# Performance work log

Measured on AMD Instinct MI355X. Metric: run time of the kernel, lower is better.

The kernel has to match this reference:

```python
import jax, jax.numpy as jnp
import numpy as np

K = 32

def leaky(v):
    return jnp.where(v >= 0, v, 0.2 * v)

def knn_cl(x, k):
    # x: [B,N,C] channel-last; returns idx [B,N,k] of k nearest (incl. self)
    xx = jnp.sum(x * x, axis=-1)                      # [B,N]
    inner = jnp.einsum('bnc,bmc->bnm', x, x)          # [B,N,N]
    pd = 2.0 * inner - xx[:, :, None] - xx[:, None, :]  # -squared dist
    return jax.lax.top_k(pd, k)[1]

def gfeat(x, k, knn_src=None):
    # x: [B,N,C] -> [B,N,k,2C] = cat(neighbor - center, center)
    idx = knn_cl(x if knn_src is None else knn_src, k)
    nb = jax.vmap(lambda f, i: f[i])(x, idx)          # [B,N,k,C]
    ctr = x[:, :, None, :]
    return jnp.concatenate([nb - ctr, jnp.broadcast_to(ctr, nb.shape)], axis=-1)

def block2(f, w, s, b):
    # 1x1 Conv2d + (folded) BN + LeakyReLU, channel-last [B,N,k,Cin]->[B,N,k,Cout]
    return leaky(jnp.einsum('bnkc,oc->bnko', f, w) * s + b)

def block1(f, w, s, b):
    # 1x1 Conv1d + (folded) BN + LeakyReLU, [B,N,Cin]->[B,N,Cout]
    return leaky(jnp.einsum('bnc,oc->bno', f, w) * s + b)

def setup_inputs() -> dict:
    key = jax.random.key(0)
    ks = jax.random.split(key, 32)
    B, C, N = 4, 8, 4096
    d = {}
    d['x'] = jax.random.normal(ks[0], (B, C, N), dtype=jnp.float32)
    wshapes = {'w1': (64, 16), 'w2': (64, 64), 'w3': (64, 128), 'w4': (64, 64),
               'w5': (64, 128), 'w6': (1024, 192), 'w7': (512, 1216),
               'w8': (256, 512), 'w9': (2, 256)}
    for i, (name, sh) in enumerate(wshapes.items()):
        d[name] = jax.random.normal(ks[1 + i], sh, dtype=jnp.float32) * 0.05
    bnsizes = [64, 64, 64, 64, 64, 1024, 512, 256]
    for i, c in enumerate(bnsizes):
        d['s%d' % (i + 1)] = jax.random.uniform(ks[10 + 2 * i], (c,), dtype=jnp.float32) + 0.5
        d['b%d' % (i + 1)] = jax.random.normal(ks[11 + 2 * i], (c,), dtype=jnp.float32) * 0.1
    return d

def reference(x, w1, w2, w3, w4, w5, w6, w7, w8, w9,
              s1, b1, s2, b2, s3, b3, s4, b4, s5, b5, s6, b6, s7, b7, s8, b8):
    B, _, N = x.shape
    xcl = jnp.transpose(x, (0, 2, 1))                 # [B,N,8]
    # EdgeConv block 1 (knn on channels 6: -> dim9=True path)
    f = gfeat(xcl, K, knn_src=xcl[..., 6:])           # [B,N,K,16]
    f = block2(f, w1, s1, b1)
    f = block2(f, w2, s2, b2)
    x1 = jnp.max(f, axis=2)                           # [B,N,64]
    # EdgeConv block 2
    f = gfeat(x1, K)                                  # [B,N,K,128]
    f = block2(f, w3, s3, b3)
    f = block2(f, w4, s4, b4)
    x2 = jnp.max(f, axis=2)                           # [B,N,64]
    # EdgeConv block 3
    f = gfeat(x2, K)                                  # [B,N,K,128]
    f = block2(f, w5, s5, b5)
    x3 = jnp.max(f, axis=2)                           # [B,N,64]
    cat = jnp.concatenate([x1, x2, x3], axis=-1)      # [B,N,192]
    g = block1(cat, w6, s6, b6)                       # [B,N,1024]
    g = jnp.broadcast_to(jnp.max(g, axis=1, keepdims=True), (B, N, 1024))
    h = jnp.concatenate([g, x1, x2, x3], axis=-1)     # [B,N,1216]
    h = block1(h, w7, s7, b7)                         # [B,N,512]
    h = block1(h, w8, s8, b8)                         # [B,N,256] (dropout is eval-mode identity)
    logits = jnp.einsum('bnc,oc->bno', h, w9)         # [B,N,2]
    return jnp.transpose(jax.nn.softmax(logits, axis=-1), (0, 2, 1))  # [B,2,N]
```

## Files before the change

### kernel.cpp

```cpp
#include <hip/hip_runtime.h>
#include <cstddef>

#define BATCH 4
#define NPTS 4096
#define KNN 32

__device__ __forceinline__ float leaky(float v) { return v >= 0.f ? v : 0.2f * v; }

__device__ __forceinline__ unsigned encf(float f) {
    unsigned b = __float_as_uint(f);
    return (b & 0x80000000u) ? ~b : (b | 0x80000000u);
}
__device__ __forceinline__ float decf(unsigned e) {
    unsigned b = (e & 0x80000000u) ? (e ^ 0x80000000u) : ~e;
    return __uint_as_float(b);
}
__device__ __forceinline__ unsigned umaxu(unsigned a, unsigned b) { return a > b ? a : b; }

__device__ __forceinline__ unsigned wave_umax_bcast(unsigned v) {
    int x = (int)v, t;
    t = __builtin_amdgcn_update_dpp(0, x, 0x111, 0xF, 0xF, true); x = (int)umaxu((unsigned)x, (unsigned)t);
    t = __builtin_amdgcn_update_dpp(0, x, 0x112, 0xF, 0xF, true); x = (int)umaxu((unsigned)x, (unsigned)t);
    t = __builtin_amdgcn_update_dpp(0, x, 0x114, 0xF, 0xF, true); x = (int)umaxu((unsigned)x, (unsigned)t);
    t = __builtin_amdgcn_update_dpp(0, x, 0x118, 0xF, 0xF, true); x = (int)umaxu((unsigned)x, (unsigned)t);
    t = __builtin_amdgcn_update_dpp(0, x, 0x142, 0xA, 0xF, true); x = (int)umaxu((unsigned)x, (unsigned)t);
    t = __builtin_amdgcn_update_dpp(0, x, 0x143, 0xC, 0xF, true); x = (int)umaxu((unsigned)x, (unsigned)t);
    return (unsigned)__builtin_amdgcn_readlane(x, 63);
}

template <int CM>
__device__ __forceinline__ void extract_step_reg(unsigned* u, unsigned* g, int lane,
                                                 int* __restrict__ outp, int it) {
    unsigned m8 = umaxu(umaxu(umaxu(g[0], g[1]), umaxu(g[2], g[3])),
                        umaxu(umaxu(g[4], g[5]), umaxu(g[6], g[7])));
    unsigned wm = wave_umax_bcast(m8);
    unsigned long long msk = __ballot(m8 == wm);
    int wl = __ffsll(msk) - 1;
    if (lane == wl) {
        int sj = -1;
        #pragma unroll
        for (int G = 0; G < 8; ++G) {
            if (sj < 0 && g[G] == wm) {
                #pragma unroll
                for (int q = 0; q < 8; ++q) {
                    if (sj < 0 && u[G * 8 + q] == wm) { u[G * 8 + q] = 0u; sj = G * 8 + q; }
                }
                unsigned ng = 0u;
                #pragma unroll
                for (int q = 0; q < 8; ++q) ng = umaxu(ng, u[G * 8 + q]);
                g[G] = ng;
            }
        }
        int col;
        if (CM == 0) col = ((sj >> 2) << 8) + (lane << 2) + (sj & 3);
        else col = (sj << 6) + lane;
        outp[it] = col;
    }
}

__global__ __launch_bounds__(256) void txcl_kernel(const float* __restrict__ x,
                                                   float* __restrict__ xcl) {
    int i = blockIdx.x * 256 + threadIdx.x;
    int n = i & 4095;
    int c = (i >> 12) & 7;
    int b = i >> 15;
    xcl[(size_t)(b * NPTS + n) * 8 + c] = x[i];
}

__global__ __launch_bounds__(256, 4) void knn1_kernel(const float* __restrict__ x,
                                                      int* __restrict__ idxo) {
    int t = threadIdx.x, w = t >> 6, lane = t & 63;
    int b = blockIdx.y;
    int row = blockIdx.x * 4 + w;
    const float* px = x + (size_t)b * 8 * NPTS + 6 * NPTS;
    const float* py = px + NPTS;
    float xr = px[row], yr = py[row];
    unsigned u[64];
    unsigned g[8];
    #pragma unroll
    for (int i = 0; i < 8; ++i) g[i] = 0u;
    #pragma unroll
    for (int j = 0; j < 64; ++j) {
        int col = (j << 6) + lane;
        float xm = px[col], ym = py[col];
        float v = 2.f * (xr * xm + yr * ym) - (xm * xm + ym * ym);
        unsigned e = encf(v);
        u[j] = e;
        g[j >> 3] = umaxu(g[j >> 3], e);
    }
    int* outp = idxo + ((size_t)(b * NPTS + row) << 5);
    for (int it = 0; it < 32; ++it)
        extract_step_reg<1>(u, g, lane, outp, it);
}

__global__ __launch_bounds__(256) void dist_gemm_kernel(const float* __restrict__ feat,
                                                        const float* __restrict__ xx,
                                                        unsigned* __restrict__ E, int b) {
    int bi = blockIdx.x >> 5, bj = blockIdx.x & 31;
    if (bi > bj) return;
    __shared__ __align__(16) float As[16][132];
    __shared__ __align__(16) float Bs[16][192];
    int t = threadIdx.x;
    int tx = t & 15, ty = t >> 4;
    const float* fb = feat + (size_t)b * NPTS * 64;
    const float* xb = xx + b * NPTS;
    int m0 = bi * 128, n0 = bj * 128;
    float acc[8][8];
    #pragma unroll
    for (int r = 0; r < 8; ++r)
        #pragma unroll
        for (int c = 0; c < 8; ++c) acc[r][c] = 0.f;
    int sm = t >> 1;
    int sk0 = (t & 1) * 8;
    int bc = (sm >> 3) * 12 + (sm & 7);
    for (int k0 = 0; k0 < 64; k0 += 16) {
        float4 a0 = *(const float4*)&fb[(size_t)(m0 + sm) * 64 + k0 + sk0];
        float4 a1 = *(const float4*)&fb[(size_t)(m0 + sm) * 64 + k0 + sk0 + 4];
        float4 b0 = *(const float4*)&fb[(size_t)(n0 + sm) * 64 + k0 + sk0];
        float4 b1 = *(const float4*)&fb[(size_t)(n0 + sm) * 64 + k0 + sk0 + 4];
        __syncthreads();
        As[sk0 + 0][sm] = a0.x; As[sk0 + 1][sm] = a0.y; As[sk0 + 2][sm] = a0.z; As[sk0 + 3][sm] = a0.w;
        As[sk0 + 4][sm] = a1.x; As[sk0 + 5][sm] = a1.y; As[sk0 + 6][sm] = a1.z; As[sk0 + 7][sm] = a1.w;
        Bs[sk0 + 0][bc] = b0.x; Bs[sk0 + 1][bc] = b0.y; Bs[sk0 + 2][bc] = b0.z; Bs[sk0 + 3][bc] = b0.w;
        Bs[sk0 + 4][bc] = b1.x; Bs[sk0 + 5][bc] = b1.y; Bs[sk0 + 6][bc] = b1.z; Bs[sk0 + 7][bc] = b1.w;
        __syncthreads();
        #pragma unroll
        for (int kk = 0; kk < 16; ++kk) {
            float4 av0 = *(const float4*)&As[kk][ty * 8];
            float4 av1 = *(const float4*)&As[kk][ty * 8 + 4];
            float4 bv0 = *(const float4*)&Bs[kk][tx * 12];
            float4 bv1 = *(const float4*)&Bs[kk][tx * 12 + 4];
            float av[8] = {av0.x, av0.y, av0.z, av0.w, av1.x, av1.y, av1.z, av1.w};
            float bv[8] = {bv0.x, bv0.y, bv0.z, bv0.w, bv1.x, bv1.y, bv1.z, bv1.w};
            #pragma unroll
            for (int r = 0; r < 8; ++r)
                #pragma unroll
                for (int c = 0; c < 8; ++c) acc[r][c] += av[r] * bv[c];
        }
    }
    float xxj[8], xxi[8];
    #pragma unroll
    for (int c = 0; c < 8; ++c) xxj[c] = xb[n0 + tx * 8 + c];
    #pragma unroll
    for (int r = 0; r < 8; ++r) xxi[r] = xb[m0 + ty * 8 + r];
    #pragma unroll
    for (int r = 0; r < 8; ++r) {
        uint4 e0, e1;
        e0.x = encf(2.f * acc[r][0] - xxj[0]); e0.y = encf(2.f * acc[r][1] - xxj[1]);
        e0.z = encf(2.f * acc[r][2] - xxj[2]); e0.w = encf(2.f * acc[r][3] - xxj[3]);
        e1.x = encf(2.f * acc[r][4] - xxj[4]); e1.y = encf(2.f * acc[r][5] - xxj[5]);
        e1.z = encf(2.f * acc[r][6] - xxj[6]); e1.w = encf(2.f * acc[r][7] - xxj[7]);
        size_t ro = ((size_t)(m0 + ty * 8 + r) << 12) + n0 + tx * 8;
        *(uint4*)&E[ro] = e0;
        *(uint4*)&E[ro + 4] = e1;
    }
    if (bi != bj) {
        #pragma unroll
        for (int c = 0; c < 8; ++c) {
            uint4 e0, e1;
            e0.x = encf(2.f * acc[0][c] - xxi[0]); e0.y = encf(2.f * acc[1][c] - xxi[1]);
            e0.z = encf(2.f * acc[2][c] - xxi[2]); e0.w = encf(2.f * acc[3][c] - xxi[3]);
            e1.x = encf(2.f * acc[4][c] - xxi[4]); e1.y = encf(2.f * acc[5][c] - xxi[5]);
            e1.z = encf(2.f * acc[6][c] - xxi[6]); e1.w = encf(2.f * acc[7][c] - xxi[7]);
            size_t ro = ((size_t)(n0 + tx * 8 + c) << 12) + m0 + ty * 8;
            *(uint4*)&E[ro] = e0;
            *(uint4*)&E[ro + 4] = e1;
        }
    }
}

__global__ __launch_bounds__(256, 4) void knn_select_kernel(const unsigned* __restrict__ E,
                                                            int* __restrict__ idxo, int b) {
    int t = threadIdx.x, w = t >> 6, lane = t & 63;
    int row = blockIdx.x * 4 + w;
    const uint4* Er = (const uint4*)(E + ((size_t)row << 12));
    unsigned u[64];
    unsigned g[8];
    #pragma unroll
    for (int i = 0; i < 8; ++i) g[i] = 0u;
    #pragma unroll
    for (int i = 0; i < 16; ++i) {
        uint4 v = Er[i * 64 + lane];
        u[4 * i + 0] = v.x;
        u[4 * i + 1] = v.y;
        u[4 * i + 2] = v.z;
        u[4 * i + 3] = v.w;
        g[i >> 1] = umaxu(g[i >> 1], umaxu(umaxu(v.x, v.y), umaxu(v.z, v.w)));
    }
    int* outp = idxo + ((size_t)(b * NPTS + row) << 5);
    for (int it = 0; it < 32; ++it)
        extract_step_reg<0>(u, g, lane, outp, it);
}

template <int KC>
__global__ __launch_bounds__(256) void qpre_kernel(const float* __restrict__ f,
                                                   const float* __restrict__ W,
                                                   float* __restrict__ P) {
    int t = threadIdx.x, w = t >> 6, lane = t & 63;
    float wlo[KC], wd[KC];
    #pragma unroll
    for (int c = 0; c < KC; c += 4) {
        float4 lo = *(const float4*)&W[lane * 2 * KC + c];
        float4 hi = *(const float4*)&W[lane * 2 * KC + KC + c];
        wlo[c] = lo.x; wlo[c + 1] = lo.y; wlo[c + 2] = lo.z; wlo[c + 3] = lo.w;
        wd[c] = hi.x - lo.x; wd[c + 1] = hi.y - lo.y; wd[c + 2] = hi.z - lo.z; wd[c + 3] = hi.w - lo.w;
    }
    int base = blockIdx.x * 32 + w * 8;
    for (int p = 0; p < 8; ++p) {
        int m = base + p;
        const float* fr = f + (size_t)m * KC;
        float alo = 0.f, ad = 0.f;
        #pragma unroll
        for (int c = 0; c < KC; c += 4) {
            float4 fv = *(const float4*)&fr[c];
            alo += wlo[c] * fv.x + wlo[c + 1] * fv.y + wlo[c + 2] * fv.z + wlo[c + 3] * fv.w;
            ad += wd[c] * fv.x + wd[c + 1] * fv.y + wd[c + 2] * fv.z + wd[c + 3] * fv.w;
        }
        P[(size_t)m * 128 + lane] = alo;
        P[(size_t)m * 128 + 64 + lane] = ad;
    }
}

__global__ __launch_bounds__(256) void edge_mm_kernel(const float* __restrict__ P,
                                                      const int* __restrict__ idx,
                                                      const float* __restrict__ sA,
                                                      const float* __restrict__ bA,
                                                      const float* __restrict__ W2,
                                                      const float* __restrict__ sB,
                                                      const float* __restrict__ bB,
                                                      float* __restrict__ xo,
                                                      float* __restrict__ xxo) {
    __shared__ __align__(16) float h1T[64][132];
    __shared__ __align__(16) float Bs[64][68];
    __shared__ __align__(16) float pdd_s[4][64];
    __shared__ float scA_s[64], biA_s[64];
    __shared__ int ids[128];
    int t = threadIdx.x;
    int b = blockIdx.y;
    int n0 = blockIdx.x * 4;
    if (t < 128) ids[t] = idx[((size_t)(b * NPTS + n0 + (t >> 5))) * KNN + (t & 31)];
    else if (t < 192) scA_s[t - 128] = sA[t - 128];
    else biA_s[t - 192] = bA[t - 192];
    pdd_s[t >> 6][t & 63] = P[((size_t)(b * NPTS + n0 + (t >> 6))) * 128 + 64 + (t & 63)];
    __syncthreads();
    {
        int o = t & 63, kk0 = (t >> 6) * 16;
        #pragma unroll
        for (int j = 0; j < 16; j += 4) {
            float4 v = *(const float4*)&W2[o * 64 + kk0 + j];
            Bs[kk0 + j + 0][o] = v.x;
            Bs[kk0 + j + 1][o] = v.y;
            Bs[kk0 + j + 2][o] = v.z;
            Bs[kk0 + j + 3][o] = v.w;
        }
    }
    #pragma unroll
    for (int p = 0; p < 2; ++p) {
        int row = p * 64 + (t >> 2);
        int w = row >> 5;
        int id = ids[row];
        int q = t & 3;
        const float* src = &P[((size_t)(b * NPTS + id)) * 128 + q * 16];
        #pragma unroll
        for (int j = 0; j < 4; ++j) {
            int c = q * 16 + j * 4;
            float4 v = *(const float4*)&src[j * 4];
            float4 sa = *(const float4*)&scA_s[c];
            float4 ba = *(const float4*)&biA_s[c];
            float4 pd = *(const float4*)&pdd_s[w][c];
            h1T[c + 0][row] = leaky(sa.x * (v.x + pd.x) + ba.x);
            h1T[c + 1][row] = leaky(sa.y * (v.y + pd.y) + ba.y);
            h1T[c + 2][row] = leaky(sa.z * (v.z + pd.z) + ba.z);
            h1T[c + 3][row] = leaky(sa.w * (v.w + pd.w) + ba.w);
        }
    }
    __syncthreads();
    int tx = t & 15, ty = t >> 4;
    float acc[8][4];
    #pragma unroll
    for (int r = 0; r < 8; ++r)
        #pragma unroll
        for (int c = 0; c < 4; ++c) acc[r][c] = 0.f;
    #pragma unroll 4
    for (int kk = 0; kk < 64; ++kk) {
        float4 a0 = *(const float4*)&h1T[kk][ty * 8];
        float4 a1 = *(const float4*)&h1T[kk][ty * 8 + 4];
        float4 bb = *(const float4*)&Bs[kk][tx * 4];
        float av[8] = {a0.x, a0.y, a0.z, a0.w, a1.x, a1.y, a1.z, a1.w};
        #pragma unroll
        for (int r = 0; r < 8; ++r) {
            acc[r][0] += av[r] * bb.x;
            acc[r][1] += av[r] * bb.y;
            acc[r][2] += av[r] * bb.z;
            acc[r][3] += av[r] * bb.w;
        }
    }
    float rm[4];
    #pragma unroll
    for (int c = 0; c < 4; ++c) {
        float m = acc[0][c];
        #pragma unroll
        for (int r = 1; r < 8; ++r) m = fmaxf(m, acc[r][c]);
        rm[c] = m;
    }
    __syncthreads();
    float (*red)[68] = Bs;
    #pragma unroll
    for (int c = 0; c < 4; ++c) red[ty][tx * 4 + c] = rm[c];
    __syncthreads();
    int w = t >> 6, lane = t & 63;
    float m = fmaxf(fmaxf(red[4 * w + 0][lane], red[4 * w + 1][lane]),
                    fmaxf(red[4 * w + 2][lane], red[4 * w + 3][lane]));
    float outv = leaky(sB[lane] * m + bB[lane]);
    xo[((size_t)(b * NPTS + n0 + w)) * 64 + lane] = outv;
    if (xxo != nullptr) {
        float sq = outv * outv;
        #pragma unroll
        for (int d = 32; d; d >>= 1) sq += __shfl_xor(sq, d, 64);
        if (lane == 0) xxo[b * NPTS + n0 + w] = sq;
    }
}

__global__ __launch_bounds__(256) void edge3_g_kernel(const float* __restrict__ P,
                                                      const int* __restrict__ idx,
                                                      const float* __restrict__ s5,
                                                      const float* __restrict__ b5,
                                                      float* __restrict__ xo) {
    int t = threadIdx.x, w = t >> 6, lane = t & 63;
    int b = blockIdx.y;
    int n = blockIdx.x * 4 + w;
    int idreg = 0;
    if (lane < 32) idreg = idx[((size_t)(b * NPTS + n)) * KNN + lane];
    float pdd = P[((size_t)(b * NPTS + n)) * 128 + 64 + lane];
    float sc = s5[lane], bi = b5[lane];
    float m = -3.402823466e38f;
    for (int k = 0; k < 32; ++k) {
        int idv = __shfl(idreg, k, 64);
        float v = P[((size_t)(b * NPTS + idv)) * 128 + lane] + pdd;
        m = fmaxf(m, leaky(sc * v + bi));
    }
    xo[((size_t)(b * NPTS + n)) * 64 + lane] = m;
}

template <int MODE>
__global__ __launch_bounds__(256) void mlp_gemm(const float* __restrict__ A1,
                                                const float* __restrict__ A2,
                                                const float* __restrict__ A3,
                                                const float* __restrict__ W,
                                                const float* __restrict__ S,
                                                const float* __restrict__ Bi,
                                                const float* __restrict__ gdotv,
                                                float* __restrict__ out,
                                                unsigned* __restrict__ outE) {
    constexpr int KD = (MODE == 2) ? 512 : 192;
    constexpr int ND = (MODE == 0) ? 1024 : (MODE == 1 ? 512 : 256);
    constexpr int WSTR = (MODE == 0) ? 192 : (MODE == 1 ? 1216 : 512);
    constexpr int WOFF = (MODE == 1) ? 1024 : 0;
    __shared__ __align__(16) float As[16][132];
    __shared__ __align__(16) float Bs[16][192];
    int t = threadIdx.x;
    int tx = t & 15, ty = t >> 4;
    int m0 = blockIdx.x * 128, n0 = blockIdx.y * 128;
    float acc[8][8];
    #pragma unroll
    for (int r = 0; r < 8; ++r)
        #pragma unroll
        for (int c = 0; c < 8; ++c) acc[r][c] = 0.f;
    int sm = t >> 1;
    int sk0 = (t & 1) * 8;
    int bc = (sm >> 3) * 12 + (sm & 7);
    for (int k0 = 0; k0 < KD; k0 += 16) {
        const float* Asrc;
        int acol;
        if (MODE == 2) {
            Asrc = A1 + (size_t)(m0 + sm) * 512;
            acol = k0 + sk0;
        } else {
            int sel = k0 >> 6;
            const float* s_ = (sel == 0) ? A1 : (sel == 1 ? A2 : A3);
            Asrc = s_ + (size_t)(m0 + sm) * 64;
            acol = (k0 & 63) + sk0;
        }
        float4 a0 = *(const float4*)&Asrc[acol];
        float4 a1 = *(const float4*)&Asrc[acol + 4];
        float4 b0 = *(const float4*)&W[(size_t)(n0 + sm) * WSTR + WOFF + k0 + sk0];
        float4 b1 = *(const float4*)&W[(size_t)(n0 + sm) * WSTR + WOFF + k0 + sk0 + 4];
        __syncthreads();
        As[sk0 + 0][sm] = a0.x; As[sk0 + 1][sm] = a0.y; As[sk0 + 2][sm] = a0.z; As[sk0 + 3][sm] = a0.w;
        As[sk0 + 4][sm] = a1.x; As[sk0 + 5][sm] = a1.y; As[sk0 + 6][sm] = a1.z; As[sk0 + 7][sm] = a1.w;
        Bs[sk0 + 0][bc] = b0.x; Bs[sk0 + 1][bc] = b0.y; Bs[sk0 + 2][bc] = b0.z; Bs[sk0 + 3][bc] = b0.w;
        Bs[sk0 + 4][bc] = b1.x; Bs[sk0 + 5][bc] = b1.y; Bs[sk0 + 6][bc] = b1.z; Bs[sk0 + 7][bc] = b1.w;
        __syncthreads();
        #pragma unroll
        for (int kk = 0; kk < 16; ++kk) {
            float4 av0 = *(const float4*)&As[kk][ty * 8];
            float4 av1 = *(const float4*)&As[kk][ty * 8 + 4];
            float4 bv0 = *(const float4*)&Bs[kk][tx * 12];
            float4 bv1 = *(const float4*)&Bs[kk][tx * 12 + 4];
            float av[8] = {av0.x, av0.y, av0.z, av0.w, av1.x, av1.y, av1.z, av1.w};
            float bv[8] = {bv0.x, bv0.y, bv0.z, bv0.w, bv1.x, bv1.y, bv1.z, bv1.w};
            #pragma unroll
            for (int r = 0; r < 8; ++r)
                #pragma unroll
                for (int c = 0; c < 8; ++c) acc[r][c] += av[r] * bv[c];
        }
    }
    int b = m0 >> 12;
    if constexpr (MODE == 0) {
        __shared__ float red[16][128];
        float pm[8];
        #pragma unroll
        for (int c = 0; c < 8; ++c) {
            int o = n0 + tx * 8 + c;
            float sc = S[o], bi = Bi[o];
            float gm = -3.402823466e38f;
            #pragma unroll
            for (int r = 0; r < 8; ++r) gm = fmaxf(gm, leaky(sc * acc[r][c] + bi));
            pm[c] = gm;
        }
        __syncthreads();
        #pragma unroll
        for (int c = 0; c < 8; ++c) red[ty][tx * 8 + c] = pm[c];
        __syncthreads();
        if (t < 128) {
            float gm = red[0][t];
            #pragma unroll
            for (int i = 1; i < 16; ++i) gm = fmaxf(gm, red[i][t]);
            atomicMax(&outE[b * 1024 + n0 + t], encf(gm));
        }
    } else {
        #pragma unroll
        for (int r = 0; r < 8; ++r) {
            int m = m0 + ty * 8 + r;
            float4 v0, v1;
            float* vp0 = (float*)&v0;
            float* vp1 = (float*)&v1;
            #pragma unroll
            for (int c = 0; c < 8; ++c) {
                int o = n0 + tx * 8 + c;
                float val = acc[r][c];
                if (MODE == 1) val += gdotv[b * 512 + o];
                float res = leaky(S[o] * val + Bi[o]);
                if (c < 4) vp0[c] = res; else vp1[c - 4] = res;
            }
            *(float4*)&out[(size_t)m * ND + n0 + tx * 8] = v0;
            *(float4*)&out[(size_t)m * ND + n0 + tx * 8 + 4] = v1;
        }
    }
}

__global__ __launch_bounds__(256) void gdot_kernel(const unsigned* __restrict__ gmaxE,
                                                   const float* __restrict__ w7,
                                                   float* __restrict__ gdotv) {
    __shared__ float gm[1024];
    int t = threadIdx.x, w = t >> 6, lane = t & 63;
    int b = blockIdx.y;
    int o = blockIdx.x * 4 + w;
    for (int i = t; i < 1024; i += 256) gm[i] = decf(gmaxE[b * 1024 + i]);
    __syncthreads();
    float a = 0.f;
    #pragma unroll
    for (int i = 0; i < 16; ++i) {
        int c = i * 64 + lane;
        a += w7[(size_t)o * 1216 + c] * gm[c];
    }
    #pragma unroll
    for (int d = 32; d; d >>= 1) a += __shfl_xor(a, d, 64);
    if (lane == 0) gdotv[b * 512 + o] = a;
}

__global__ __launch_bounds__(256) void final_kernel(const float* __restrict__ h256,
                                                    const float* __restrict__ w9,
                                                    float* __restrict__ outp) {
    int t = threadIdx.x, w = t >> 6, lane = t & 63;
    int b = blockIdx.y;
    int n = blockIdx.x * 4 + w;
    const float* h = h256 + (size_t)(b * NPTS + n) * 256;
    float a0 = 0.f, a1 = 0.f;
    #pragma unroll
    for (int i = 0; i < 4; ++i) {
        int c = i * 64 + lane;
        float hv = h[c];
        a0 += w9[c] * hv;
        a1 += w9[256 + c] * hv;
    }
    #pragma unroll
    for (int d = 32; d; d >>= 1) {
        a0 += __shfl_xor(a0, d, 64);
        a1 += __shfl_xor(a1, d, 64);
    }
    if (lane == 0) {
        float m = fmaxf(a0, a1);
        float e0 = expf(a0 - m), e1 = expf(a1 - m);
        float s = e0 + e1;
        outp[(size_t)b * 2 * NPTS + n] = e0 / s;
        outp[(size_t)b * 2 * NPTS + NPTS + n] = e1 / s;
    }
}

extern "C" void kernel_launch(void* const* d_in, const int* in_sizes, int n_in,
                              void* d_out, int out_size, void* d_ws, size_t ws_size,
                              hipStream_t stream) {
    (void)in_sizes; (void)n_in; (void)out_size; (void)ws_size;
    const float* x = (const float*)d_in[0];
    const float* w1 = (const float*)d_in[1];
    const float* w2 = (const float*)d_in[2];
    const float* w3 = (const float*)d_in[3];
    const float* w4 = (const float*)d_in[4];
    const float* w5 = (const float*)d_in[5];
    const float* w6 = (const float*)d_in[6];
    const float* w7 = (const float*)d_in[7];
    const float* w8 = (const float*)d_in[8];
    const float* w9 = (const float*)d_in[9];
    const float* s1 = (const float*)d_in[10]; const float* b1 = (const float*)d_in[11];
    const float* s2 = (const float*)d_in[12]; const float* b2 = (const float*)d_in[13];
    const float* s3 = (const float*)d_in[14]; const float* b3 = (const float*)d_in[15];
    const float* s4 = (const float*)d_in[16]; const float* b4 = (const float*)d_in[17];
    const float* s5 = (const float*)d_in[18]; const float* b5 = (const float*)d_in[19];
    const float* s6 = (const float*)d_in[20]; const float* b6 = (const float*)d_in[21];
    const float* s7 = (const float*)d_in[22]; const float* b7 = (const float*)d_in[23];
    const float* s8 = (const float*)d_in[24]; const float* b8 = (const float*)d_in[25];
    float* out = (float*)d_out;

    float* xcl = (float*)d_ws;
    float* x1 = xcl + 131072;
    float* x2 = x1 + 1048576;
    float* x3 = x2 + 1048576;
    float* xxA = x3 + 1048576;
    float* xxB = xxA + 16384;
    float* gdotv = xxB + 16384;
    unsigned* gmaxE = (unsigned*)(gdotv + 2048);
    int* idx1 = (int*)(gmaxE + 4096);
    int* idx2 = idx1 + 524288;
    int* idx3 = idx2 + 524288;
    float* t512 = (float*)(idx3 + 524288);
    float* h256 = t512 + 8388608;
    unsigned* Ebuf = (unsigned*)(h256 + 4194304);
    float* Pbuf = t512;

    hipMemsetAsync(gmaxE, 0, 4096 * sizeof(unsigned), stream);

    txcl_kernel<<<512, 256, 0, stream>>>(x, xcl);
    knn1_kernel<<<dim3(1024, 4), 256, 0, stream>>>(x, idx1);
    qpre_kernel<8><<<512, 256, 0, stream>>>(xcl, w1, Pbuf);
    edge_mm_kernel<<<dim3(1024, 4), 256, 0, stream>>>(Pbuf, idx1, s1, b1, w2, s2, b2, x1, xxA);
    for (int b = 0; b < 4; ++b) {
        dist_gemm_kernel<<<1024, 256, 0, stream>>>(x1, xxA, Ebuf, b);
        knn_select_kernel<<<1024, 256, 0, stream>>>(Ebuf, idx2, b);
    }
    qpre_kernel<64><<<512, 256, 0, stream>>>(x1, w3, Pbuf);
    edge_mm_kernel<<<dim3(1024, 4), 256, 0, stream>>>(Pbuf, idx2, s3, b3, w4, s4, b4, x2, xxB);
    for (int b = 0; b < 4; ++b) {
        dist_gemm_kernel<<<1024, 256, 0, stream>>>(x2, xxB, Ebuf, b);
        knn_select_kernel<<<1024, 256, 0, stream>>>(Ebuf, idx3, b);
    }
    qpre_kernel<64><<<512, 256, 0, stream>>>(x2, w5, Pbuf);
    edge3_g_kernel<<<dim3(1024, 4), 256, 0, stream>>>(Pbuf, idx3, s5, b5, x3);
    mlp_gemm<0><<<dim3(128, 8), 256, 0, stream>>>(x1, x2, x3, w6, s6, b6, nullptr, nullptr, gmaxE);
    gdot_kernel<<<dim3(128, 4), 256, 0, stream>>>(gmaxE, w7, gdotv);
    mlp_gemm<1><<<dim3(128, 4), 256, 0, stream>>>(x1, x2, x3, w7, s7, b7, gdotv, t512, nullptr);
    mlp_gemm<2><<<dim3(128, 2), 256, 0, stream>>>(t512, nullptr, nullptr, w8, s8, b8, nullptr, h256, nullptr);
    final_kernel<<<dim3(1024, 4), 256, 0, stream>>>(h256, w9, out);
}
```

Baseline: 1.071 ms.

## Batch kNN distance/select over all batches; streamline top-k extraction and edge3 max

The per-batch loop of dist_gemm and knn_select launches is replaced by a single launch of each over a 4-deep grid, with a separate distance buffer per batch. This applies only when the workspace is large enough, so the GPU gets four times more blocks per launch and there are fewer launch gaps. The top-k extraction keeps a running wave maximum between steps and finds the matching group and element with bitmask ffs instead of sequential guarded searches. In edge3, the affine BN and leaky activation are hoisted out of the neighbor max, which relies on positive scales for monotonicity. The batched path needs a much larger workspace and writes more memory traffic at once.

```diff
diff --git a/kernel.cpp b/kernel.cpp
--- a/kernel.cpp
+++ b/kernel.cpp
@@ -29,31 +29,38 @@
 }
 
 template <int CM>
-__device__ __forceinline__ void extract_step_reg(unsigned* u, unsigned* g, int lane,
-                                                 int* __restrict__ outp, int it) {
-    unsigned m8 = umaxu(umaxu(umaxu(g[0], g[1]), umaxu(g[2], g[3])),
-                        umaxu(umaxu(g[4], g[5]), umaxu(g[6], g[7])));
+__device__ __forceinline__ void extract_step_reg(unsigned* u, unsigned* g, unsigned& m8,
+                                                 int lane, int* __restrict__ outp, int it) {
     unsigned wm = wave_umax_bcast(m8);
     unsigned long long msk = __ballot(m8 == wm);
     int wl = __ffsll(msk) - 1;
     if (lane == wl) {
-        int sj = -1;
+        unsigned gmask = 0;
+        #pragma unroll
+        for (int G = 0; G < 8; ++G) gmask |= (g[G] == wm ? 1u : 0u) << G;
+        int gi = __ffs(gmask) - 1;
+        int sq = 0;
         #pragma unroll
         for (int G = 0; G < 8; ++G) {
-            if (sj < 0 && g[G] == wm) {
+            if (G == gi) {
+                unsigned qm = 0;
                 #pragma unroll
-                for (int q = 0; q < 8; ++q) {
-                    if (sj < 0 && u[G * 8 + q] == wm) { u[G * 8 + q] = 0u; sj = G * 8 + q; }
-                }
-                unsigned ng = 0u;
+                for (int q = 0; q < 8; ++q) qm |= (u[G * 8 + q] == wm ? 1u : 0u) << q;
+                int q0 = __ffs(qm) - 1;
+                #pragma unroll
+                for (int q = 0; q < 8; ++q) u[G * 8 + q] = (q == q0) ? 0u : u[G * 8 + q];
+                unsigned ng = 0;
                 #pragma unroll
                 for (int q = 0; q < 8; ++q) ng = umaxu(ng, u[G * 8 + q]);
                 g[G] = ng;
+                sq = G * 8 + q0;
             }
         }
+        m8 = umaxu(umaxu(umaxu(g[0], g[1]), umaxu(g[2], g[3])),
+                   umaxu(umaxu(g[4], g[5]), umaxu(g[6], g[7])));
         int col;
-        if (CM == 0) col = ((sj >> 2) << 8) + (lane << 2) + (sj & 3);
-        else col = (sj << 6) + lane;
+        if (CM == 0) col = ((sq >> 2) << 8) + (lane << 2) + (sq & 3);
+        else col = (sq << 6) + lane;
         outp[it] = col;
     }
 }
@@ -88,16 +95,21 @@
         u[j] = e;
         g[j >> 3] = umaxu(g[j >> 3], e);
     }
+    unsigned m8 = umaxu(umaxu(umaxu(g[0], g[1]), umaxu(g[2], g[3])),
+                        umaxu(umaxu(g[4], g[5]), umaxu(g[6], g[7])));
     int* outp = idxo + ((size_t)(b * NPTS + row) << 5);
     for (int it = 0; it < 32; ++it)
-        extract_step_reg<1>(u, g, lane, outp, it);
+        extract_step_reg<1>(u, g, m8, lane, outp, it);
 }
 
 __global__ __launch_bounds__(256) void dist_gemm_kernel(const float* __restrict__ feat,
                                                         const float* __restrict__ xx,
-                                                        unsigned* __restrict__ E, int b) {
+                                                        unsigned* __restrict__ E0,
+                                                        int b0, unsigned long long estride) {
     int bi = blockIdx.x >> 5, bj = blockIdx.x & 31;
     if (bi > bj) return;
+    unsigned* E = E0 + (size_t)blockIdx.y * estride;
+    int b = b0 + blockIdx.y;
     __shared__ __align__(16) float As[16][132];
     __shared__ __align__(16) float Bs[16][192];
     int t = threadIdx.x;
@@ -116,13 +128,13 @@
     for (int k0 = 0; k0 < 64; k0 += 16) {
         float4 a0 = *(const float4*)&fb[(size_t)(m0 + sm) * 64 + k0 + sk0];
         float4 a1 = *(const float4*)&fb[(size_t)(m0 + sm) * 64 + k0 + sk0 + 4];
-        float4 b0 = *(const float4*)&fb[(size_t)(n0 + sm) * 64 + k0 + sk0];
-        float4 b1 = *(const float4*)&fb[(size_t)(n0 + sm) * 64 + k0 + sk0 + 4];
+        float4 b0v = *(const float4*)&fb[(size_t)(n0 + sm) * 64 + k0 + sk0];
+        float4 b1v = *(const float4*)&fb[(size_t)(n0 + sm) * 64 + k0 + sk0 + 4];
         __syncthreads();
         As[sk0 + 0][sm] = a0.x; As[sk0 + 1][sm] = a0.y; As[sk0 + 2][sm] = a0.z; As[sk0 + 3][sm] = a0.w;
         As[sk0 + 4][sm] = a1.x; As[sk0 + 5][sm] = a1.y; As[sk0 + 6][sm] = a1.z; As[sk0 + 7][sm] = a1.w;
-        Bs[sk0 + 0][bc] = b0.x; Bs[sk0 + 1][bc] = b0.y; Bs[sk0 + 2][bc] = b0.z; Bs[sk0 + 3][bc] = b0.w;
-        Bs[sk0 + 4][bc] = b1.x; Bs[sk0 + 5][bc] = b1.y; Bs[sk0 + 6][bc] = b1.z; Bs[sk0 + 7][bc] = b1.w;
+        Bs[sk0 + 0][bc] = b0v.x; Bs[sk0 + 1][bc] = b0v.y; Bs[sk0 + 2][bc] = b0v.z; Bs[sk0 + 3][bc] = b0v.w;
+        Bs[sk0 + 4][bc] = b1v.x; Bs[sk0 + 5][bc] = b1v.y; Bs[sk0 + 6][bc] = b1v.z; Bs[sk0 + 7][bc] = b1v.w;
         __syncthreads();
         #pragma unroll
         for (int kk = 0; kk < 16; ++kk) {
@@ -169,8 +181,11 @@
     }
 }
 
-__global__ __launch_bounds__(256, 4) void knn_select_kernel(const unsigned* __restrict__ E,
-                                                            int* __restrict__ idxo, int b) {
+__global__ __launch_bounds__(256, 4) void knn_select_kernel(const unsigned* __restrict__ E0,
+                                                            int* __restrict__ idxo,
+                                                            int b0, unsigned long long estride) {
+    const unsigned* E = E0 + (size_t)blockIdx.y * estride;
+    int b = b0 + blockIdx.y;
     int t = threadIdx.x, w = t >> 6, lane = t & 63;
     int row = blockIdx.x * 4 + w;
     const uint4* Er = (const uint4*)(E + ((size_t)row << 12));
@@ -187,9 +202,11 @@
         u[4 * i + 3] = v.w;
         g[i >> 1] = umaxu(g[i >> 1], umaxu(umaxu(v.x, v.y), umaxu(v.z, v.w)));
     }
+    unsigned m8 = umaxu(umaxu(umaxu(g[0], g[1]), umaxu(g[2], g[3])),
+                        umaxu(umaxu(g[4], g[5]), umaxu(g[6], g[7])));
     int* outp = idxo + ((size_t)(b * NPTS + row) << 5);
     for (int it = 0; it < 32; ++it)
-        extract_step_reg<0>(u, g, lane, outp, it);
+        extract_step_reg<0>(u, g, m8, lane, outp, it);
 }
 
 template <int KC>
@@ -336,10 +353,9 @@
     float m = -3.402823466e38f;
     for (int k = 0; k < 32; ++k) {
         int idv = __shfl(idreg, k, 64);
-        float v = P[((size_t)(b * NPTS + idv)) * 128 + lane] + pdd;
-        m = fmaxf(m, leaky(sc * v + bi));
-    }
-    xo[((size_t)(b * NPTS + n)) * 64 + lane] = m;
+        m = fmaxf(m, P[((size_t)(b * NPTS + idv)) * 128 + lane]);
+    }
+    xo[((size_t)(b * NPTS + n)) * 64 + lane] = leaky(sc * (m + pdd) + bi);
 }
 
 template <int MODE>
@@ -501,7 +517,7 @@
 extern "C" void kernel_launch(void* const* d_in, const int* in_sizes, int n_in,
                               void* d_out, int out_size, void* d_ws, size_t ws_size,
                               hipStream_t stream) {
-    (void)in_sizes; (void)n_in; (void)out_size; (void)ws_size;
+    (void)in_sizes; (void)n_in; (void)out_size;
     const float* x = (const float*)d_in[0];
     const float* w1 = (const float*)d_in[1];
     const float* w2 = (const float*)d_in[2];
@@ -538,21 +554,35 @@
     unsigned* Ebuf = (unsigned*)(h256 + 4194304);
     float* Pbuf = t512;
 
+    const unsigned long long ESTR = 16777216ull;
+    size_t need4 = (17471488ull + 4ull * ESTR) * 4ull;
+    bool batched = ws_size >= need4;
+
     hipMemsetAsync(gmaxE, 0, 4096 * sizeof(unsigned), stream);
 
     txcl_kernel<<<512, 256, 0, stream>>>(x, xcl);
     knn1_kernel<<<dim3(1024, 4), 256, 0, stream>>>(x, idx1);
     qpre_kernel<8><<<512, 256, 0, stream>>>(xcl, w1, Pbuf);
     edge_mm_kernel<<<dim3(1024, 4), 256, 0, stream>>>(Pbuf, idx1, s1, b1, w2, s2, b2, x1, xxA);
-    for (int b = 0; b < 4; ++b) {
-        dist_gemm_kernel<<<1024, 256, 0, stream>>>(x1, xxA, Ebuf, b);
-        knn_select_kernel<<<1024, 256, 0, stream>>>(Ebuf, idx2, b);
+    if (batched) {
+        dist_gemm_kernel<<<dim3(1024, 4), 256, 0, stream>>>(x1, xxA, Ebuf, 0, ESTR);
+        knn_select_kernel<<<dim3(1024, 4), 256, 0, stream>>>(Ebuf, idx2, 0, ESTR);
+    } else {
+        for (int b = 0; b < 4; ++b) {
+            dist_gemm_kernel<<<dim3(1024, 1), 256, 0, stream>>>(x1, xxA, Ebuf, b, 0);
+            knn_select_kernel<<<dim3(1024, 1), 256, 0, stream>>>(Ebuf, idx2, b, 0);
+        }
     }
     qpre_kernel<64><<<512, 256, 0, stream>>>(x1, w3, Pbuf);
     edge_mm_kernel<<<dim3(1024, 4), 256, 0, stream>>>(Pbuf, idx2, s3, b3, w4, s4, b4, x2, xxB);
-    for (int b = 0; b < 4; ++b) {
-        dist_gemm_kernel<<<1024, 256, 0, stream>>>(x2, xxB, Ebuf, b);
-        knn_select_kernel<<<1024, 256, 0, stream>>>(Ebuf, idx3, b);
+    if (batched) {
+        dist_gemm_kernel<<<dim3(1024, 4), 256, 0, stream>>>(x2, xxB, Ebuf, 0, ESTR);
+        knn_select_kernel<<<dim3(1024, 4), 256, 0, stream>>>(Ebuf, idx3, 0, ESTR);
+    } else {
+        for (int b = 0; b < 4; ++b) {
+            dist_gemm_kernel<<<dim3(1024, 1), 256, 0, stream>>>(x2, xxB, Ebuf, b, 0);
+            knn_select_kernel<<<dim3(1024, 1), 256, 0, stream>>>(Ebuf, idx3, b, 0);
+        }
     }
     qpre_kernel<64><<<512, 256, 0, stream>>>(x2, w5, Pbuf);
     edge3_g_kernel<<<dim3(1024, 4), 256, 0, stream>>>(Pbuf, idx3, s5, b5, x3);
```

Result: slower. 1.114 ms (+4.1%).
